# Kernel optimization log

Measured on AMD Instinct MI355X. Metric: run time of the kernel, lower is better.

## Reference

```python
import jax, jax.numpy as jnp
import numpy as np

IN_FEATURES = 2048
OUT_FEATURES = 2048
TOP_K = 1024


def setup_inputs() -> dict:
    key = jax.random.key(0)
    kx, kw, kb = jax.random.split(key, 3)
    bound = 1.0 / np.sqrt(IN_FEATURES)
    x = jax.random.normal(kx, (8, 2048, IN_FEATURES), dtype=jnp.float32)
    weight = jax.random.uniform(kw, (OUT_FEATURES, IN_FEATURES), dtype=jnp.float32,
                                minval=-bound, maxval=bound)
    bias = jax.random.uniform(kb, (OUT_FEATURES,), dtype=jnp.float32,
                              minval=-bound, maxval=bound)
    return {"x": x, "weight": weight, "bias": bias}


def _topk_mask(weight: jnp.ndarray, k: int) -> jnp.ndarray:
    # Per output row, keep the k largest-magnitude weights (binary mask).
    _, idx = jax.lax.top_k(jnp.abs(weight), k)            # [out, k]
    rows = jnp.arange(weight.shape[0])[:, None]            # [out, 1]
    mask = jnp.zeros_like(weight).at[rows, idx].set(1.0)   # scatter ones
    return mask


def reference(x, weight, bias):
    # y = x @ (mask * W)^T + b, mask = top-k by |W| per output feature
    mask = _topk_mask(weight, TOP_K)
    masked_weight = weight * mask                          # [out, in]
    return jnp.einsum('bsi,oi->bso', x, masked_weight) + bias
```

## Files before the change

kernel.cpp:

```cpp
#include <hip/hip_runtime.h>

typedef __attribute__((ext_vector_type(8))) short s16x8;
typedef __attribute__((ext_vector_type(4))) float f32x4;
typedef __attribute__((ext_vector_type(8))) unsigned short u16x8;

#define GLB(p) ((const __attribute__((address_space(1))) void*)(p))
#define LDS(p) ((__attribute__((address_space(3))) void*)(p))

#define BAR() __builtin_amdgcn_s_barrier()
#define LGKM(n) asm volatile("s_waitcnt lgkmcnt(" #n ")" ::: "memory")
#define VMC(n) asm volatile("s_waitcnt vmcnt(" #n ")" ::: "memory")

__device__ __forceinline__ unsigned short f2bf(float f) {
  unsigned u = __float_as_uint(f);
  u += 0x7fffu + ((u >> 16) & 1u);
  return (unsigned short)(u >> 16);
}

__global__ __launch_bounds__(256) void prep_kernel(
    const float* __restrict__ W, unsigned short* __restrict__ Wb,
    const float* __restrict__ X, unsigned short* __restrict__ Xb) {
  __shared__ int hist[4096];
  __shared__ int scanres[2];
  __shared__ int wsum[4];
  const int tid  = threadIdx.x;

  if (blockIdx.x >= 2048) {
    const size_t i = ((size_t)(blockIdx.x - 2048) * 256 + tid) * 8;
    const float4* xp = (const float4*)(X + i);
    const float4 a = xp[0], b = xp[1];
    u16x8 o;
    o[0] = f2bf(a.x); o[1] = f2bf(a.y); o[2] = f2bf(a.z); o[3] = f2bf(a.w);
    o[4] = f2bf(b.x); o[5] = f2bf(b.y); o[6] = f2bf(b.z); o[7] = f2bf(b.w);
    *(u16x8*)(Xb + i) = o;
    return;
  }

  const int lane = tid & 63;
  const int wv   = tid >> 6;
  const int row  = blockIdx.x;
  const float* wr = W + (size_t)row * 2048;

  const float4 v0 = *(const float4*)(wr + tid * 8);
  const float4 v1 = *(const float4*)(wr + tid * 8 + 4);
  float val[8] = {v0.x, v0.y, v0.z, v0.w, v1.x, v1.y, v1.z, v1.w};
  unsigned key[8];
#pragma unroll
  for (int e = 0; e < 8; ++e) key[e] = __float_as_uint(val[e]) & 0x7fffffffu;

  unsigned prefix = 0;
  int rem = 1024;

  for (int i = tid; i < 4096; i += 256) hist[i] = 0;
  __syncthreads();
#pragma unroll
  for (int e = 0; e < 8; ++e) atomicAdd(&hist[key[e] >> 20], 1);
  __syncthreads();
  if (wv == 0) {
    const int base = 4096 - (lane + 1) * 64;
    int s = 0;
    for (int b = 0; b < 64; ++b) s += hist[base + b];
    int cum = s;
#pragma unroll
    for (int off = 1; off < 64; off <<= 1) {
      int o = __shfl_up(cum, off, 64);
      if (lane >= off) cum += o;
    }
    const int cumex = cum - s;
    if (cumex < rem && rem <= cum) {
      int running = cumex;
      for (int b = 63; b >= 0; --b) {
        int h = hist[base + b];
        if (running + h >= rem) { scanres[0] = base + b; scanres[1] = rem - running; break; }
        running += h;
      }
    }
  }
  __syncthreads();
  prefix = ((unsigned)scanres[0]) << 20;
  rem = scanres[1];
  __syncthreads();

  for (int i = tid; i < 1024; i += 256) hist[i] = 0;
  __syncthreads();
#pragma unroll
  for (int e = 0; e < 8; ++e)
    if ((key[e] >> 20) == (prefix >> 20)) atomicAdd(&hist[(key[e] >> 10) & 1023], 1);
  __syncthreads();
  if (wv == 0) {
    const int base = 1024 - (lane + 1) * 16;
    int s = 0;
    for (int b = 0; b < 16; ++b) s += hist[base + b];
    int cum = s;
#pragma unroll
    for (int off = 1; off < 64; off <<= 1) {
      int o = __shfl_up(cum, off, 64);
      if (lane >= off) cum += o;
    }
    const int cumex = cum - s;
    if (cumex < rem && rem <= cum) {
      int running = cumex;
      for (int b = 15; b >= 0; --b) {
        int h = hist[base + b];
        if (running + h >= rem) { scanres[0] = base + b; scanres[1] = rem - running; break; }
        running += h;
      }
    }
  }
  __syncthreads();
  prefix |= ((unsigned)scanres[0]) << 10;
  rem = scanres[1];
  __syncthreads();

  for (int i = tid; i < 1024; i += 256) hist[i] = 0;
  __syncthreads();
#pragma unroll
  for (int e = 0; e < 8; ++e)
    if ((key[e] >> 10) == (prefix >> 10)) atomicAdd(&hist[key[e] & 1023], 1);
  __syncthreads();
  if (wv == 0) {
    const int base = 1024 - (lane + 1) * 16;
    int s = 0;
    for (int b = 0; b < 16; ++b) s += hist[base + b];
    int cum = s;
#pragma unroll
    for (int off = 1; off < 64; off <<= 1) {
      int o = __shfl_up(cum, off, 64);
      if (lane >= off) cum += o;
    }
    const int cumex = cum - s;
    if (cumex < rem && rem <= cum) {
      int running = cumex;
      for (int b = 15; b >= 0; --b) {
        int h = hist[base + b];
        if (running + h >= rem) { scanres[0] = base + b; scanres[1] = rem - running; break; }
        running += h;
      }
    }
  }
  __syncthreads();
  const unsigned T = prefix | (unsigned)scanres[0];
  rem = scanres[1];

  int eqcnt = 0;
#pragma unroll
  for (int e = 0; e < 8; ++e) eqcnt += (key[e] == T) ? 1 : 0;
  int c = eqcnt;
#pragma unroll
  for (int off = 1; off < 64; off <<= 1) {
    int o = __shfl_up(c, off, 64);
    if (lane >= off) c += o;
  }
  if (lane == 63) wsum[wv] = c;
  __syncthreads();
  int wavebase = 0;
  for (int j = 0; j < wv; ++j) wavebase += wsum[j];
  const int myex = wavebase + c - eqcnt;

  u16x8 o;
  int r = 0;
#pragma unroll
  for (int e = 0; e < 8; ++e) {
    const bool iseq = (key[e] == T);
    const bool keep = (key[e] > T) || (iseq && (myex + r) < rem);
    r += iseq ? 1 : 0;
    o[e] = keep ? f2bf(val[e]) : (unsigned short)0;
  }
  *(u16x8*)(Wb + (size_t)row * 2048 + tid * 8) = o;
}

__global__ __launch_bounds__(512, 2) void gemm_bt_kernel(
    const unsigned short* __restrict__ A,
    const unsigned short* __restrict__ B,
    const float* __restrict__ bias,
    float* __restrict__ C) {
  constexpr int K = 2048;
  constexpr int N = 2048;
  constexpr int T = K / 64;
  constexpr size_t HK = (size_t)128 * K;

  __shared__ __align__(16) char lds_[131072];

  const int tid = threadIdx.x;
  const int l   = tid & 63;
  const int wv  = tid >> 6;
  const int wm  = wv & 1;
  const int wn  = wv >> 1;

  const int lin = blockIdx.x;
  const int o   = (lin & 7) * 64 + (lin >> 3);
  const int tm  = o >> 3;
  const int tn  = o & 7;

  int rS[2], cS[2];
#pragma unroll
  for (int e = 0; e < 2; ++e) {
    const int d   = (e * 512 + tid) * 16;
    const int off = d ^ (((d >> 9) & 1) << 5);
    rS[e] = ((off >> 11) << 4) | ((off >> 6) & 15);
    cS[e] = (((off >> 10) & 1) << 5) | (((off >> 4) & 3) << 3);
  }
  const unsigned short* const pA0 = A + (size_t)(tm * 256 + rS[0]) * K + cS[0];
  const unsigned short* const pA1 = A + (size_t)(tm * 256 + rS[1]) * K + cS[1];
  const unsigned short* const pB0 = B + (size_t)(tn * 256 + rS[0]) * K + cS[0];
  const unsigned short* const pB1 = B + (size_t)(tn * 256 + rS[1]) * K + cS[1];

  auto stage = [&](const unsigned short* g0, const unsigned short* g1, char* d) {
    __builtin_amdgcn_global_load_lds(GLB(g0), LDS(d + wv * 1024), 16, 0, 0);
    __builtin_amdgcn_global_load_lds(GLB(g1), LDS(d + 8192 + wv * 1024), 16, 0, 0);
  };

  const int laneoff = (((l & 15) << 6) | ((l >> 4) << 4)) ^ ((l & 8) << 2);
  const char* const aRd = (const char*)lds_ + wm * 2048 + laneoff;
  const char* const bRd = (const char*)lds_ + 65536 + wn * 2048 + laneoff;

  f32x4 acc[8][4] = {};

  stage(pA0,            pA1,            lds_);
  stage(pB0 + HK,       pB1 + HK,       lds_ + 65536 + 16384);
  stage(pA0 + HK,       pA1 + HK,       lds_ + 16384);
  stage(pB0,            pB1,            lds_ + 65536);
  stage(pA0 + 64,       pA1 + 64,       lds_ + 32768);
  stage(pB0 + HK + 64,  pB1 + HK + 64,  lds_ + 65536 + 32768 + 16384);
  stage(pA0 + HK + 64,  pA1 + HK + 64,  lds_ + 32768 + 16384);
  VMC(6);
  BAR();

  for (int t = 0; t < T; ++t) {
    const int bb = t & 1;
    const char* aT = aRd + bb * 32768;
    const char* bT = bRd + bb * 32768;
    char* sA  = lds_ + bb * 32768;
    char* sB  = lds_ + 65536 + bb * 32768;
    char* sBn = lds_ + 65536 + (bb ^ 1) * 32768;

    s16x8 af[4][2], f0[2][2], f1[2][2];

#pragma unroll
    for (int i = 0; i < 4; ++i) {
      af[i][0] = *(const s16x8*)(aT + i * 4096);
      af[i][1] = *(const s16x8*)(aT + i * 4096 + 1024);
    }
#pragma unroll
    for (int j = 0; j < 2; ++j) {
      f0[j][0] = *(const s16x8*)(bT + j * 8192);
      f0[j][1] = *(const s16x8*)(bT + j * 8192 + 1024);
    }
    if (t + 1 < T)
      stage(pB0 + (size_t)(t + 1) * 64, pB1 + (size_t)(t + 1) * 64, sBn);
    LGKM(8);
    BAR();
    LGKM(0);
    __builtin_amdgcn_s_setprio(1);
#pragma unroll
    for (int kk = 0; kk < 2; ++kk)
#pragma unroll
      for (int i = 0; i < 4; ++i)
#pragma unroll
        for (int j = 0; j < 2; ++j)
          acc[i][j] = __builtin_amdgcn_mfma_f32_16x16x32_bf16(af[i][kk], f0[j][kk], acc[i][j], 0, 0, 0);
    __builtin_amdgcn_s_setprio(0);
    BAR();

#pragma unroll
    for (int j = 0; j < 2; ++j) {
      f1[j][0] = *(const s16x8*)(bT + 16384 + j * 8192);
      f1[j][1] = *(const s16x8*)(bT + 16384 + j * 8192 + 1024);
    }
    if (t + 2 < T)
      stage(pA0 + (size_t)(t + 2) * 64, pA1 + (size_t)(t + 2) * 64, sA);
    BAR();
    LGKM(0);
    __builtin_amdgcn_s_setprio(1);
#pragma unroll
    for (int kk = 0; kk < 2; ++kk)
#pragma unroll
      for (int i = 0; i < 4; ++i)
#pragma unroll
        for (int j = 0; j < 2; ++j)
          acc[i][j + 2] = __builtin_amdgcn_mfma_f32_16x16x32_bf16(af[i][kk], f1[j][kk], acc[i][j + 2], 0, 0, 0);
    __builtin_amdgcn_s_setprio(0);
    BAR();

#pragma unroll
    for (int i = 0; i < 4; ++i) {
      af[i][0] = *(const s16x8*)(aT + 16384 + i * 4096);
      af[i][1] = *(const s16x8*)(aT + 16384 + i * 4096 + 1024);
    }
    if (t + 2 < T)
      stage(pB0 + HK + (size_t)(t + 2) * 64, pB1 + HK + (size_t)(t + 2) * 64, sB + 16384);
    BAR();
    LGKM(0);
    __builtin_amdgcn_s_setprio(1);
#pragma unroll
    for (int kk = 0; kk < 2; ++kk)
#pragma unroll
      for (int i = 0; i < 4; ++i)
#pragma unroll
        for (int j = 0; j < 2; ++j)
          acc[i + 4][j + 2] = __builtin_amdgcn_mfma_f32_16x16x32_bf16(af[i][kk], f1[j][kk], acc[i + 4][j + 2], 0, 0, 0);
    __builtin_amdgcn_s_setprio(0);
    BAR();

#pragma unroll
    for (int j = 0; j < 2; ++j) {
      f0[j][0] = *(const s16x8*)(bT + j * 8192);
      f0[j][1] = *(const s16x8*)(bT + j * 8192 + 1024);
    }
    if (t + 2 < T)
      stage(pA0 + HK + (size_t)(t + 2) * 64, pA1 + HK + (size_t)(t + 2) * 64, sA + 16384);
    BAR();
    LGKM(0);
    __builtin_amdgcn_s_setprio(1);
#pragma unroll
    for (int kk = 0; kk < 2; ++kk)
#pragma unroll
      for (int i = 0; i < 4; ++i)
#pragma unroll
        for (int j = 0; j < 2; ++j)
          acc[i + 4][j] = __builtin_amdgcn_mfma_f32_16x16x32_bf16(af[i][kk], f0[j][kk], acc[i + 4][j], 0, 0, 0);
    __builtin_amdgcn_s_setprio(0);
    if (t + 2 < T) { VMC(6); } else { VMC(0); }
    BAR();
  }

  float bv[4];
#pragma unroll
  for (int j = 0; j < 4; ++j)
    bv[j] = bias[tn * 256 + (4 * j + wn) * 16 + (l & 15)];

  const int crow0 = tm * 256 + wm * 16 + (l >> 4) * 4;
  const int ccol0 = tn * 256 + wn * 16 + (l & 15);
  float* Cp = C + (size_t)crow0 * N + ccol0;
#pragma unroll
  for (int i = 0; i < 8; ++i)
#pragma unroll
    for (int j = 0; j < 4; ++j)
#pragma unroll
      for (int r = 0; r < 4; ++r)
        Cp[(size_t)(i * 32 + r) * N + j * 64] = acc[i][j][r] + bv[j];
}

extern "C" void kernel_launch(void* const* d_in, const int* in_sizes, int n_in,
                              void* d_out, int out_size, void* d_ws, size_t ws_size,
                              hipStream_t stream) {
  const float* x    = (const float*)d_in[0];
  const float* w    = (const float*)d_in[1];
  const float* bias = (const float*)d_in[2];
  float* out = (float*)d_out;

  constexpr int M = 8 * 2048;
  constexpr int N = 2048;
  constexpr int K = 2048;

  unsigned short* xb = (unsigned short*)d_ws;
  unsigned short* wb = xb + (size_t)M * K;

  const int conv_blocks = ((size_t)M * K) / (256 * 8);
  prep_kernel<<<2048 + conv_blocks, 256, 0, stream>>>(w, wb, x, xb);
  gemm_bt_kernel<<<(M / 256) * (N / 256), 512, 0, stream>>>(xb, wb, bias, out);
}
```

Baseline: 356.7 us.

## Restructure GEMM main loop to cut barriers and reorder LDS fragment loads

Reworks the per-iteration schedule of the bf16 MFMA GEMM loop. It removes the explicit lgkmcnt waits and several barriers, and loads the high B fragments in the first phase so they are reused across two MFMA blocks. The next-A and low-B fragment reads are now placed right after the MFMA blocks, before the barriers. The aim is fewer workgroup synchronisation points and more overlap of LDS reads with MFMA. Dropping barriers changes the ordering between async global-to-LDS stages and fragment reads, which risks read-after-write hazards and makes correctness depend on the compiler's own waitcnt insertion.

```diff
diff --git a/kernel.cpp b/kernel.cpp
--- a/kernel.cpp
+++ b/kernel.cpp
@@ -8,7 +8,6 @@
 #define LDS(p) ((__attribute__((address_space(3))) void*)(p))
 
 #define BAR() __builtin_amdgcn_s_barrier()
-#define LGKM(n) asm volatile("s_waitcnt lgkmcnt(" #n ")" ::: "memory")
 #define VMC(n) asm volatile("s_waitcnt vmcnt(" #n ")" ::: "memory")
 
 __device__ __forceinline__ unsigned short f2bf(float f) {
@@ -234,23 +233,27 @@
     char* sB  = lds_ + 65536 + bb * 32768;
     char* sBn = lds_ + 65536 + (bb ^ 1) * 32768;
 
-    s16x8 af[4][2], f0[2][2], f1[2][2];
-
-#pragma unroll
-    for (int i = 0; i < 4; ++i) {
-      af[i][0] = *(const s16x8*)(aT + i * 4096);
-      af[i][1] = *(const s16x8*)(aT + i * 4096 + 1024);
-    }
-#pragma unroll
-    for (int j = 0; j < 2; ++j) {
-      f0[j][0] = *(const s16x8*)(bT + j * 8192);
-      f0[j][1] = *(const s16x8*)(bT + j * 8192 + 1024);
-    }
+    s16x8 af[4][2], bLo[2][2], bHi[2][2];
+
     if (t + 1 < T)
       stage(pB0 + (size_t)(t + 1) * 64, pB1 + (size_t)(t + 1) * 64, sBn);
-    LGKM(8);
-    BAR();
-    LGKM(0);
+#pragma unroll
+    for (int i = 0; i < 4; ++i)
+      af[i][0] = *(const s16x8*)(aT + i * 4096);
+#pragma unroll
+    for (int j = 0; j < 2; ++j)
+      bLo[j][0] = *(const s16x8*)(bT + j * 8192);
+#pragma unroll
+    for (int i = 0; i < 4; ++i)
+      af[i][1] = *(const s16x8*)(aT + i * 4096 + 1024);
+#pragma unroll
+    for (int j = 0; j < 2; ++j)
+      bLo[j][1] = *(const s16x8*)(bT + j * 8192 + 1024);
+#pragma unroll
+    for (int j = 0; j < 2; ++j) {
+      bHi[j][0] = *(const s16x8*)(bT + 16384 + j * 8192);
+      bHi[j][1] = *(const s16x8*)(bT + 16384 + j * 8192 + 1024);
+    }
     __builtin_amdgcn_s_setprio(1);
 #pragma unroll
     for (int kk = 0; kk < 2; ++kk)
@@ -258,19 +261,12 @@
       for (int i = 0; i < 4; ++i)
 #pragma unroll
         for (int j = 0; j < 2; ++j)
-          acc[i][j] = __builtin_amdgcn_mfma_f32_16x16x32_bf16(af[i][kk], f0[j][kk], acc[i][j], 0, 0, 0);
+          acc[i][j] = __builtin_amdgcn_mfma_f32_16x16x32_bf16(af[i][kk], bLo[j][kk], acc[i][j], 0, 0, 0);
     __builtin_amdgcn_s_setprio(0);
     BAR();
 
-#pragma unroll
-    for (int j = 0; j < 2; ++j) {
-      f1[j][0] = *(const s16x8*)(bT + 16384 + j * 8192);
-      f1[j][1] = *(const s16x8*)(bT + 16384 + j * 8192 + 1024);
-    }
     if (t + 2 < T)
       stage(pA0 + (size_t)(t + 2) * 64, pA1 + (size_t)(t + 2) * 64, sA);
-    BAR();
-    LGKM(0);
     __builtin_amdgcn_s_setprio(1);
 #pragma unroll
     for (int kk = 0; kk < 2; ++kk)
@@ -278,39 +274,35 @@
       for (int i = 0; i < 4; ++i)
 #pragma unroll
         for (int j = 0; j < 2; ++j)
-          acc[i][j + 2] = __builtin_amdgcn_mfma_f32_16x16x32_bf16(af[i][kk], f1[j][kk], acc[i][j + 2], 0, 0, 0);
+          acc[i][j + 2] = __builtin_amdgcn_mfma_f32_16x16x32_bf16(af[i][kk], bHi[j][kk], acc[i][j + 2], 0, 0, 0);
     __builtin_amdgcn_s_setprio(0);
-    BAR();
-
 #pragma unroll
     for (int i = 0; i < 4; ++i) {
       af[i][0] = *(const s16x8*)(aT + 16384 + i * 4096);
       af[i][1] = *(const s16x8*)(aT + 16384 + i * 4096 + 1024);
     }
+    BAR();
+
     if (t + 2 < T)
       stage(pB0 + HK + (size_t)(t + 2) * 64, pB1 + HK + (size_t)(t + 2) * 64, sB + 16384);
+    __builtin_amdgcn_s_setprio(1);
+#pragma unroll
+    for (int kk = 0; kk < 2; ++kk)
+#pragma unroll
+      for (int i = 0; i < 4; ++i)
+#pragma unroll
+        for (int j = 0; j < 2; ++j)
+          acc[i + 4][j + 2] = __builtin_amdgcn_mfma_f32_16x16x32_bf16(af[i][kk], bHi[j][kk], acc[i + 4][j + 2], 0, 0, 0);
+    __builtin_amdgcn_s_setprio(0);
+#pragma unroll
+    for (int j = 0; j < 2; ++j) {
+      bLo[j][0] = *(const s16x8*)(bT + j * 8192);
+      bLo[j][1] = *(const s16x8*)(bT + j * 8192 + 1024);
+    }
     BAR();
-    LGKM(0);
-    __builtin_amdgcn_s_setprio(1);
-#pragma unroll
-    for (int kk = 0; kk < 2; ++kk)
-#pragma unroll
-      for (int i = 0; i < 4; ++i)
-#pragma unroll
-        for (int j = 0; j < 2; ++j)
-          acc[i + 4][j + 2] = __builtin_amdgcn_mfma_f32_16x16x32_bf16(af[i][kk], f1[j][kk], acc[i + 4][j + 2], 0, 0, 0);
-    __builtin_amdgcn_s_setprio(0);
-    BAR();
-
-#pragma unroll
-    for (int j = 0; j < 2; ++j) {
-      f0[j][0] = *(const s16x8*)(bT + j * 8192);
-      f0[j][1] = *(const s16x8*)(bT + j * 8192 + 1024);
-    }
+
     if (t + 2 < T)
       stage(pA0 + HK + (size_t)(t + 2) * 64, pA1 + HK + (size_t)(t + 2) * 64, sA + 16384);
-    BAR();
-    LGKM(0);
     __builtin_amdgcn_s_setprio(1);
 #pragma unroll
     for (int kk = 0; kk < 2; ++kk)
@@ -318,7 +310,7 @@
       for (int i = 0; i < 4; ++i)
 #pragma unroll
         for (int j = 0; j < 2; ++j)
-          acc[i + 4][j] = __builtin_amdgcn_mfma_f32_16x16x32_bf16(af[i][kk], f0[j][kk], acc[i + 4][j], 0, 0, 0);
+          acc[i + 4][j] = __builtin_amdgcn_mfma_f32_16x16x32_bf16(af[i][kk], bLo[j][kk], acc[i + 4][j], 0, 0, 0);
     __builtin_amdgcn_s_setprio(0);
     if (t + 2 < T) { VMC(6); } else { VMC(0); }
     BAR();
```

Result: no change. 351.4 us (-1.5%).
